# Performance work log

Measured on AMD Instinct MI355X. Metric: run time of the kernel, lower is better.

## Reference

```python
import jax, jax.numpy as jnp
import numpy as np

EPS = 1e-5

def layernorm(x, g, b):
    mu = jnp.mean(x, axis=-1, keepdims=True)
    var = jnp.mean(jnp.square(x - mu), axis=-1, keepdims=True)
    return (x - mu) * jax.lax.rsqrt(var + EPS) * g + b

def setup_inputs() -> dict:
    key = jax.random.key(0)
    ks = jax.random.split(key, 12)
    B, V, P, C = 2, 8192, 16, 256
    FFN_IN, FFN_HID = 2 * C, 2 * C * 4
    s = 0.02
    return {
        "source": jax.random.normal(ks[0], (B, V, C), jnp.float32),
        "target": jax.random.normal(ks[1], (B, V, P, C), jnp.float32),
        "weights": jax.random.uniform(ks[2], (B, V, P), jnp.float32),
        "confidences": jax.random.uniform(ks[3], (B, V, P), jnp.float32),
        "Wq": jax.random.normal(ks[4], (C, C), jnp.float32) * s,
        "Wk": jax.random.normal(ks[5], (C, C), jnp.float32) * s,
        "Wv": jax.random.normal(ks[6], (C, C), jnp.float32) * s,
        "Wm": jax.random.normal(ks[7], (C, C), jnp.float32) * s,
        "g1": jnp.ones((C,), jnp.float32),
        "b1": jnp.zeros((C,), jnp.float32),
        "Wf1": jax.random.normal(ks[8], (FFN_IN, FFN_HID), jnp.float32) * s,
        "Wf2": jax.random.normal(ks[9], (FFN_HID, C), jnp.float32) * s,
        "g2": jnp.ones((C,), jnp.float32),
        "b2": jnp.zeros((C,), jnp.float32),
    }

NUM_HEAD = 8

def reference(source, target, weights, confidences, Wq, Wk, Wv, Wm, g1, b1, Wf1, Wf2, g2, b2):
    B, V, P, C = target.shape
    H = NUM_HEAD
    D = C // H
    # projections (bias-free linears)
    q = (source @ Wq).reshape(B, V, H, D)          # [B,V,H,D]
    k = (target @ Wk).reshape(B, V, P, H, D)       # [B,V,P,H,D]
    v = (target @ Wv).reshape(B, V, P, H, D)
    # scores scaled by per-neighbor weights then softmax over P
    scores = jnp.einsum("bvhd,bvphd->bvhp", q, k) * weights[:, :, None, :] / jnp.sqrt(jnp.float32(D))
    attn = jax.nn.softmax(scores, axis=-1)          # [B,V,H,P]
    # confidence-scaled weighted sum over neighbors
    out = jnp.einsum("bvhp,bvp,bvphd->bvhd", attn, confidences, v).reshape(B, V, C)
    message = layernorm(out @ Wm, g1, b1)
    h = jnp.concatenate([source, message], axis=-1) @ Wf1
    message = layernorm(jax.nn.gelu(h, approximate=False) @ Wf2, g2, b2)
    return source + message
```

## Files before the change

### kernel.cpp

```cpp
#include <hip/hip_runtime.h>
#include <hip/hip_bf16.h>
#include <math.h>

#define T_TOK 16384
#define CC 256
#define PP 16
#define HH 8
#define DD 32
#define LN_EPS 1e-5f

typedef __attribute__((ext_vector_type(8))) short bf16x8_t;
typedef __attribute__((ext_vector_type(4))) float f32x4_t;

__device__ __forceinline__ unsigned short f2bf(float x) {
  __hip_bfloat16 h = __float2bfloat16(x);
  return *reinterpret_cast<unsigned short*>(&h);
}
__device__ __forceinline__ float bf2f(unsigned short u) {
  union { unsigned int i; float f; } v; v.i = ((unsigned int)u) << 16; return v.f;
}
__device__ __forceinline__ void gl_lds16(const unsigned short* g, unsigned short* l) {
  __builtin_amdgcn_global_load_lds(
      (const __attribute__((address_space(1))) unsigned int*)g,
      (__attribute__((address_space(3))) unsigned int*)l, 16, 0, 0);
}

__global__ __launch_bounds__(256) void cvt_bf16_kernel(const float* __restrict__ src,
                                                       unsigned short* __restrict__ dst) {
  int i = (blockIdx.x * 256 + threadIdx.x) * 4;
  float4 v = *(const float4*)&src[i];
  ushort4 o = make_ushort4(f2bf(v.x), f2bf(v.y), f2bf(v.z), f2bf(v.w));
  *(ushort4*)&dst[i] = o;
}

__global__ __launch_bounds__(256) void transpose_cvt_kernel(const float* __restrict__ src,
                                                            unsigned short* __restrict__ dst,
                                                            int K, int N) {
  __shared__ float tile[64][65];
  int k0 = blockIdx.x * 64, n0 = blockIdx.y * 64;
  int tid = threadIdx.x;
#pragma unroll
  for (int i = 0; i < 16; i++) {
    int lin = i * 256 + tid, r = lin >> 6, c = lin & 63;
    tile[r][c] = src[(size_t)(k0 + r) * N + n0 + c];
  }
  __syncthreads();
#pragma unroll
  for (int i = 0; i < 16; i++) {
    int lin = i * 256 + tid, n = lin >> 6, k = lin & 63;
    dst[(size_t)(n0 + n) * K + k0 + k] = f2bf(tile[k][n]);
  }
}

__global__ __launch_bounds__(256) void precM_kernel(const float* __restrict__ Wq,
                                                    const float* __restrict__ Wk,
                                                    unsigned short* __restrict__ Mt) {
  __shared__ float wqS[256][33];
  __shared__ float wkS[128][33];
  const int tid = threadIdx.x;
  const int h = blockIdx.x >> 1, eh = blockIdx.x & 1;
#pragma unroll
  for (int it = 0; it < 32; it++) {
    int lin = it * 256 + tid, r = lin >> 5, d = lin & 31;
    wqS[r][d] = Wq[(size_t)r * CC + h * DD + d];
  }
#pragma unroll
  for (int it = 0; it < 16; it++) {
    int lin = it * 256 + tid, r = lin >> 5, d = lin & 31;
    wkS[r][d] = Wk[(size_t)(eh * 128 + r) * CC + h * DD + d];
  }
  __syncthreads();
  const int w = tid >> 6, l = tid & 63;
  for (int ei = 0; ei < 32; ei++) {
    int e = w * 32 + ei;
    float o[4] = {0.f, 0.f, 0.f, 0.f};
#pragma unroll
    for (int d = 0; d < 32; d++) {
      float kv = wkS[e][d];
      o[0] += kv * wqS[l][d];
      o[1] += kv * wqS[l + 64][d];
      o[2] += kv * wqS[l + 128][d];
      o[3] += kv * wqS[l + 192][d];
    }
    size_t rowb = (size_t)(h * 256 + eh * 128 + e) * CC;
    Mt[rowb + l] = f2bf(o[0]);
    Mt[rowb + l + 64] = f2bf(o[1]);
    Mt[rowb + l + 128] = f2bf(o[2]);
    Mt[rowb + l + 192] = f2bf(o[3]);
  }
}

__global__ __launch_bounds__(256) void precWVM_kernel(const float* __restrict__ Wv,
                                                      const float* __restrict__ Wm,
                                                      unsigned short* __restrict__ WVMt) {
  __shared__ float WvS[256][33];
  __shared__ float WmS[32][257];
  const int h = blockIdx.x;
  const int tid = threadIdx.x;
#pragma unroll
  for (int it = 0; it < 32; it++) {
    int lin = it * 256 + tid, e = lin >> 5, d = lin & 31;
    WvS[e][d] = Wv[(size_t)e * CC + h * DD + d];
  }
#pragma unroll
  for (int it = 0; it < 32; it++) {
    int lin = it * 256 + tid, d = lin >> 8, c = lin & 255;
    WmS[d][c] = Wm[(size_t)(h * DD + d) * CC + c];
  }
  __syncthreads();
  float wm[32];
#pragma unroll
  for (int d = 0; d < 32; d++) wm[d] = WmS[d][tid];
  for (int e = 0; e < 256; e++) {
    float acc = 0.f;
#pragma unroll
    for (int d = 0; d < 32; d++) acc += WvS[e][d] * wm[d];
    WVMt[(size_t)tid * 2048 + h * 256 + e] = f2bf(acc);
  }
}

__global__ __launch_bounds__(512) void qk_gemm_kernel(
    const unsigned short* __restrict__ A, const unsigned short* __restrict__ Bt,
    unsigned short* __restrict__ Out, int K, int strideO) {
  __shared__ __align__(16) unsigned short As[64 * 32];
  __shared__ __align__(16) unsigned short Bs[256 * 32];
  const int tid = threadIdx.x;
  const int wv = tid >> 6, l = tid & 63;
  const int wr = wv >> 2, wc = wv & 3;
  const int lr = l & 15, lq = l >> 4;
  const int m0 = blockIdx.x * 64;
  const int n0 = blockIdx.y * 256;
  const int nsteps = K >> 5;

  f32x4_t acc[2][4];
#pragma unroll
  for (int m = 0; m < 2; m++)
#pragma unroll
    for (int n = 0; n < 4; n++) acc[m][n] = (f32x4_t){0.f, 0.f, 0.f, 0.f};

  const int rA = tid >> 2, sA = tid & 3, qA = sA ^ ((rA >> 1) & 3);

  for (int st = 0; st < nsteps; st++) {
    int kn = st * 32;
    if (tid < 256) gl_lds16(&A[(size_t)(m0 + rA) * K + kn + qA * 8], &As[tid * 8]);
#pragma unroll
    for (int it = 0; it < 2; it++) {
      int lin = it * 512 + tid, r = lin >> 2, s = lin & 3, q = s ^ ((r >> 1) & 3);
      gl_lds16(&Bt[(size_t)(n0 + r) * K + kn + q * 8], &Bs[lin * 8]);
    }
    __syncthreads();
    bf16x8_t af[2], bfr[4];
#pragma unroll
    for (int m = 0; m < 2; m++) {
      int r = wr * 32 + m * 16 + lr;
      int s = lq ^ ((r >> 1) & 3);
      af[m] = *(const bf16x8_t*)&As[r * 32 + s * 8];
    }
#pragma unroll
    for (int n = 0; n < 4; n++) {
      int r = wc * 64 + n * 16 + lr;
      int s = lq ^ ((r >> 1) & 3);
      bfr[n] = *(const bf16x8_t*)&Bs[r * 32 + s * 8];
    }
#pragma unroll
    for (int m = 0; m < 2; m++)
#pragma unroll
      for (int n = 0; n < 4; n++)
        acc[m][n] = __builtin_amdgcn_mfma_f32_16x16x32_bf16(af[m], bfr[n], acc[m][n], 0, 0, 0);
    __syncthreads();
  }

#pragma unroll
  for (int m = 0; m < 2; m++)
#pragma unroll
    for (int n = 0; n < 4; n++)
#pragma unroll
      for (int j = 0; j < 4; j++) {
        int rl = wr * 32 + m * 16 + lq * 4 + j;
        int col = n0 + wc * 64 + n * 16 + lr;
        Out[(size_t)(m0 + rl) * strideO + col] = f2bf(acc[m][n][j]);
      }
}

__global__ __launch_bounds__(256) void attn2_kernel(const unsigned short* __restrict__ QKc,
                                                    const float* __restrict__ target,
                                                    const float* __restrict__ wts,
                                                    const float* __restrict__ conf,
                                                    unsigned short* __restrict__ TC) {
  __shared__ __align__(16) unsigned short Ts[4][16 * 256];
  __shared__ float awL[4][PP][HH];
  const int tid = threadIdx.x;
  const int w = tid >> 6, l = tid & 63;
  const int t = blockIdx.x * 4 + w;
  const float* trow = target + (size_t)t * PP * CC;
  char* tsb = (char*)&Ts[w][0];

  {
    const int p = l >> 2;
#pragma unroll
    for (int i = 0; i < 8; i++) {
      int s = (l & 3) + i * 4;
      const float* gp = &trow[p * CC + s * 8];
      float4 v0 = *(const float4*)gp;
      float4 v1 = *(const float4*)(gp + 4);
      ushort4 u0 = make_ushort4(f2bf(v0.x), f2bf(v0.y), f2bf(v0.z), f2bf(v0.w));
      ushort4 u1 = make_ushort4(f2bf(v1.x), f2bf(v1.y), f2bf(v1.z), f2bf(v1.w));
      uint4 pk;
      pk.x = (unsigned)u0.x | ((unsigned)u0.y << 16);
      pk.y = (unsigned)u0.z | ((unsigned)u0.w << 16);
      pk.z = (unsigned)u1.x | ((unsigned)u1.y << 16);
      pk.w = (unsigned)u1.z | ((unsigned)u1.w << 16);
      *(uint4*)(tsb + p * 512 + ((s ^ (p & 7)) << 4)) = pk;
    }
  }

  f32x4_t sc4 = (f32x4_t){0.f, 0.f, 0.f, 0.f};
  {
    const int lr = l & 15, lq = l >> 4;
    const unsigned short* qkrow = QKc + (size_t)t * 2048 + (size_t)(lr & 7) * 256;
#pragma unroll
    for (int es = 0; es < 8; es++) {
      int slot = es * 4 + lq;
      bf16x8_t aF = *(const bf16x8_t*)(tsb + lr * 512 + ((slot ^ (lr & 7)) << 4));
      bf16x8_t bF = *(const bf16x8_t*)&qkrow[es * 32 + lq * 8];
      sc4 = __builtin_amdgcn_mfma_f32_16x16x32_bf16(aF, bF, sc4, 0, 0, 0);
    }
  }

  {
    const int g = l >> 4;
    const float rsD = 0.17677669529663687f;
    float sc[4], cf[4];
#pragma unroll
    for (int j = 0; j < 4; j++) {
      int p = g * 4 + j;
      sc[j] = sc4[j] * wts[(size_t)t * PP + p] * rsD;
      cf[j] = conf[(size_t)t * PP + p];
    }
    float mx = fmaxf(fmaxf(sc[0], sc[1]), fmaxf(sc[2], sc[3]));
    mx = fmaxf(mx, __shfl_xor(mx, 16, 64));
    mx = fmaxf(mx, __shfl_xor(mx, 32, 64));
    float ex[4], sm = 0.f;
#pragma unroll
    for (int j = 0; j < 4; j++) { ex[j] = expf(sc[j] - mx); sm += ex[j]; }
    sm += __shfl_xor(sm, 16, 64);
    sm += __shfl_xor(sm, 32, 64);
    float inv = 1.f / sm;
    if ((l & 15) < 8) {
#pragma unroll
      for (int j = 0; j < 4; j++) awL[w][g * 4 + j][l & 15] = ex[j] * inv * cf[j];
    }
  }

  float tc[HH][4];
#pragma unroll
  for (int h = 0; h < HH; h++)
#pragma unroll
    for (int j = 0; j < 4; j++) tc[h][j] = 0.f;
#pragma unroll
  for (int p = 0; p < PP; p++) {
    uint2 tv = *(const uint2*)(tsb + p * 512 + (((l >> 1) ^ (p & 7)) << 4) + (l & 1) * 8);
    float te0 = bf2f((unsigned short)(tv.x & 0xffff));
    float te1 = bf2f((unsigned short)(tv.x >> 16));
    float te2 = bf2f((unsigned short)(tv.y & 0xffff));
    float te3 = bf2f((unsigned short)(tv.y >> 16));
#pragma unroll
    for (int h = 0; h < HH; h++) {
      float a = awL[w][p][h];
      tc[h][0] += a * te0; tc[h][1] += a * te1;
      tc[h][2] += a * te2; tc[h][3] += a * te3;
    }
  }
  size_t tcb = (size_t)t * 2048;
#pragma unroll
  for (int h = 0; h < HH; h++) {
    ushort4 o = make_ushort4(f2bf(tc[h][0]), f2bf(tc[h][1]), f2bf(tc[h][2]), f2bf(tc[h][3]));
    *(ushort4*)&TC[tcb + h * 2048 / HH + 4 * l] = o;
  }
}

template<int EPI>
__global__ __launch_bounds__(256) void nwide_gemm_kernel(
    const unsigned short* __restrict__ A, const unsigned short* __restrict__ Bt,
    unsigned short* __restrict__ OutB, float* __restrict__ OutF,
    const float* __restrict__ gam, const float* __restrict__ bet,
    const float* __restrict__ res) {
  __shared__ __align__(16) unsigned short As[32 * 32];
  __shared__ __align__(16) unsigned short Bs[256 * 32];
  __shared__ float redS[32][5], redQ[32][5];
  const int tid = threadIdx.x;
  const int wc = tid >> 6, l = tid & 63;
  const int lr = l & 15, lq = l >> 4;
  const int m0 = blockIdx.x * 32;
  const int K = 2048;

  f32x4_t acc[2][4];
#pragma unroll
  for (int m = 0; m < 2; m++)
#pragma unroll
    for (int n = 0; n < 4; n++) acc[m][n] = (f32x4_t){0.f, 0.f, 0.f, 0.f};

  const int rA = tid >> 2, sA = tid & 3, qA = sA ^ ((rA >> 1) & 3);

  for (int st = 0; st < 64; st++) {
    int kn = st * 32;
    if (tid < 128) gl_lds16(&A[(size_t)(m0 + rA) * K + kn + qA * 8], &As[tid * 8]);
#pragma unroll
    for (int it = 0; it < 4; it++) {
      int lin = it * 256 + tid, r = lin >> 2, s = lin & 3, q = s ^ ((r >> 1) & 3);
      gl_lds16(&Bt[(size_t)r * K + kn + q * 8], &Bs[lin * 8]);
    }
    __syncthreads();
    bf16x8_t af[2], bfr[4];
#pragma unroll
    for (int m = 0; m < 2; m++) {
      int r = m * 16 + lr;
      int s = lq ^ ((r >> 1) & 3);
      af[m] = *(const bf16x8_t*)&As[r * 32 + s * 8];
    }
#pragma unroll
    for (int n = 0; n < 4; n++) {
      int r = wc * 64 + n * 16 + lr;
      int s = lq ^ ((r >> 1) & 3);
      bfr[n] = *(const bf16x8_t*)&Bs[r * 32 + s * 8];
    }
#pragma unroll
    for (int m = 0; m < 2; m++)
#pragma unroll
      for (int n = 0; n < 4; n++)
        acc[m][n] = __builtin_amdgcn_mfma_f32_16x16x32_bf16(af[m], bfr[n], acc[m][n], 0, 0, 0);
    __syncthreads();
  }

  float s1[2][4], s2[2][4];
#pragma unroll
  for (int m = 0; m < 2; m++)
#pragma unroll
    for (int j = 0; j < 4; j++) {
      float a = 0.f, b = 0.f;
#pragma unroll
      for (int n = 0; n < 4; n++) { float x = acc[m][n][j]; a += x; b += x * x; }
      s1[m][j] = a; s2[m][j] = b;
    }
#pragma unroll
  for (int mask = 1; mask < 16; mask <<= 1)
#pragma unroll
    for (int m = 0; m < 2; m++)
#pragma unroll
      for (int j = 0; j < 4; j++) {
        s1[m][j] += __shfl_xor(s1[m][j], mask, 64);
        s2[m][j] += __shfl_xor(s2[m][j], mask, 64);
      }
  if (lr == 0) {
#pragma unroll
    for (int m = 0; m < 2; m++)
#pragma unroll
      for (int j = 0; j < 4; j++) {
        int rl = m * 16 + lq * 4 + j;
        redS[rl][wc] = s1[m][j];
        redQ[rl][wc] = s2[m][j];
      }
  }
  __syncthreads();
#pragma unroll
  for (int m = 0; m < 2; m++)
#pragma unroll
    for (int j = 0; j < 4; j++) {
      int rl = m * 16 + lq * 4 + j;
      float ts = redS[rl][0] + redS[rl][1] + redS[rl][2] + redS[rl][3];
      float tq = redQ[rl][0] + redQ[rl][1] + redQ[rl][2] + redQ[rl][3];
      float mu = ts * (1.f / 256.f);
      float var = tq * (1.f / 256.f) - mu * mu;
      float rs = rsqrtf(var + LN_EPS);
      size_t rowg = (size_t)(m0 + rl);
#pragma unroll
      for (int n = 0; n < 4; n++) {
        int col = wc * 64 + n * 16 + lr;
        float v = (acc[m][n][j] - mu) * rs * gam[col] + bet[col];
        if constexpr (EPI == 0) {
          OutB[rowg * CC + col] = f2bf(v);
        } else {
          OutF[rowg * CC + col] = res[rowg * CC + col] + v;
        }
      }
    }
}

__global__ __launch_bounds__(256) void gemm1_kernel(
    const unsigned short* __restrict__ SB, const unsigned short* __restrict__ MSG,
    const unsigned short* __restrict__ W1t, unsigned short* __restrict__ hid) {
  __shared__ __align__(16) unsigned short As[128 * 32];
  __shared__ __align__(16) unsigned short Bs[128 * 32];
  const int tid = threadIdx.x;
  const int wv = tid >> 6, l = tid & 63;
  const int wr = wv >> 1, wc = wv & 1;
  const int lr = l & 15, lq = l >> 4;
  const int m0 = blockIdx.x * 128;
  const int n0 = blockIdx.y * 128;

  f32x4_t acc[4][4];
#pragma unroll
  for (int m = 0; m < 4; m++)
#pragma unroll
    for (int n = 0; n < 4; n++) acc[m][n] = (f32x4_t){0.f, 0.f, 0.f, 0.f};

  for (int st = 0; st < 16; st++) {
    int kn = st * 32;
#pragma unroll
    for (int it = 0; it < 2; it++) {
      int lin = it * 256 + tid, r = lin >> 2, s = lin & 3, q = s ^ ((r >> 1) & 3);
      int ka = kn + q * 8;
      const unsigned short* ap = (ka < 256) ? &SB[(size_t)(m0 + r) * CC + ka]
                                            : &MSG[(size_t)(m0 + r) * CC + ka - 256];
      gl_lds16(ap, &As[lin * 8]);
      gl_lds16(&W1t[(size_t)(n0 + r) * 512 + kn + q * 8], &Bs[lin * 8]);
    }
    __syncthreads();
    bf16x8_t af[4], bf[4];
#pragma unroll
    for (int m = 0; m < 4; m++) {
      int r = wr * 64 + m * 16 + lr;
      int s = lq ^ ((r >> 1) & 3);
      af[m] = *(const bf16x8_t*)&As[r * 32 + s * 8];
    }
#pragma unroll
    for (int n = 0; n < 4; n++) {
      int r = wc * 64 + n * 16 + lr;
      int s = lq ^ ((r >> 1) & 3);
      bf[n] = *(const bf16x8_t*)&Bs[r * 32 + s * 8];
    }
#pragma unroll
    for (int m = 0; m < 4; m++)
#pragma unroll
      for (int n = 0; n < 4; n++)
        acc[m][n] = __builtin_amdgcn_mfma_f32_16x16x32_bf16(af[m], bf[n], acc[m][n], 0, 0, 0);
    __syncthreads();
  }

#pragma unroll
  for (int m = 0; m < 4; m++)
#pragma unroll
    for (int n = 0; n < 4; n++)
#pragma unroll
      for (int j = 0; j < 4; j++) {
        int row = m0 + wr * 64 + m * 16 + lq * 4 + j;
        int col = n0 + wc * 64 + n * 16 + lr;
        float x = acc[m][n][j];
        float gl = 0.5f * x * (1.0f + erff(x * 0.70710678118654752f));
        hid[(size_t)row * 2048 + col] = f2bf(gl);
      }
}

extern "C" void kernel_launch(void* const* d_in, const int* in_sizes, int n_in,
                              void* d_out, int out_size, void* d_ws, size_t ws_size,
                              hipStream_t stream) {
  const float* source = (const float*)d_in[0];
  const float* target = (const float*)d_in[1];
  const float* weights = (const float*)d_in[2];
  const float* conf   = (const float*)d_in[3];
  const float* Wq = (const float*)d_in[4];
  const float* Wk = (const float*)d_in[5];
  const float* Wv = (const float*)d_in[6];
  const float* Wm = (const float*)d_in[7];
  const float* g1 = (const float*)d_in[8];
  const float* b1 = (const float*)d_in[9];
  const float* Wf1 = (const float*)d_in[10];
  const float* Wf2 = (const float*)d_in[11];
  const float* g2 = (const float*)d_in[12];
  const float* b2 = (const float*)d_in[13];
  float* out = (float*)d_out;

  unsigned short* SB   = (unsigned short*)d_ws;
  unsigned short* MSGb = SB + (size_t)T_TOK * CC;
  unsigned short* Mt   = MSGb + (size_t)T_TOK * CC;
  unsigned short* WVMt = Mt + (size_t)2048 * 256;
  unsigned short* WF1t = WVMt + (size_t)256 * 2048;
  unsigned short* WF2t = WF1t + (size_t)2048 * 512;
  unsigned short* BIG1 = WF2t + (size_t)256 * 2048;
  unsigned short* BIG2 = BIG1 + (size_t)T_TOK * 2048;
  unsigned short* QKc  = BIG1;
  unsigned short* hid  = BIG1;
  unsigned short* TC   = BIG2;

  cvt_bf16_kernel<<<T_TOK * CC / 1024, 256, 0, stream>>>(source, SB);
  transpose_cvt_kernel<<<dim3(8, 32), 256, 0, stream>>>(Wf1, WF1t, 512, 2048);
  transpose_cvt_kernel<<<dim3(32, 4), 256, 0, stream>>>(Wf2, WF2t, 2048, 256);
  precM_kernel<<<16, 256, 0, stream>>>(Wq, Wk, Mt);
  precWVM_kernel<<<8, 256, 0, stream>>>(Wv, Wm, WVMt);

  qk_gemm_kernel<<<dim3(T_TOK / 64, 8), 512, 0, stream>>>(SB, Mt, QKc, 256, 2048);
  attn2_kernel<<<T_TOK / 4, 256, 0, stream>>>(QKc, target, weights, conf, TC);
  nwide_gemm_kernel<0><<<T_TOK / 32, 256, 0, stream>>>(
      TC, WVMt, MSGb, nullptr, g1, b1, nullptr);

  gemm1_kernel<<<dim3(T_TOK / 128, 16), 256, 0, stream>>>(SB, MSGb, WF1t, hid);
  nwide_gemm_kernel<1><<<T_TOK / 32, 256, 0, stream>>>(
      hid, WF2t, nullptr, out, g2, b2, source);
}
```

Baseline: 359.7 us.

## Double-buffer LDS tiles in the three GEMM kernels to overlap loads with MFMA

Converts the qk, nwide and gemm1 GEMM main loops to ping-pong LDS buffers, prefetching the next K-slice via global_load_lds while MFMAs consume the current one, with a prologue load of the first slice. This targets the exposed global-load latency of the single-buffered load→sync→compute→sync loop. It doubles LDS use per block, which can lower occupancy, and relies on the remaining end-of-iteration barrier to keep the buffers safe. A TC store index is also rewritten to an equivalent constant form.

```diff
diff --git a/kernel.cpp b/kernel.cpp
--- a/kernel.cpp
+++ b/kernel.cpp
@@ -122,8 +122,8 @@
 __global__ __launch_bounds__(512) void qk_gemm_kernel(
     const unsigned short* __restrict__ A, const unsigned short* __restrict__ Bt,
     unsigned short* __restrict__ Out, int K, int strideO) {
-  __shared__ __align__(16) unsigned short As[64 * 32];
-  __shared__ __align__(16) unsigned short Bs[256 * 32];
+  __shared__ __align__(16) unsigned short As[2][64 * 32];
+  __shared__ __align__(16) unsigned short Bs[2][256 * 32];
   const int tid = threadIdx.x;
   const int wv = tid >> 6, l = tid & 63;
   const int wr = wv >> 2, wc = wv & 3;
@@ -140,27 +140,37 @@
 
   const int rA = tid >> 2, sA = tid & 3, qA = sA ^ ((rA >> 1) & 3);
 
+  if (tid < 256) gl_lds16(&A[(size_t)(m0 + rA) * K + qA * 8], &As[0][tid * 8]);
+#pragma unroll
+  for (int it = 0; it < 2; it++) {
+    int lin = it * 512 + tid, r = lin >> 2, s = lin & 3, q = s ^ ((r >> 1) & 3);
+    gl_lds16(&Bt[(size_t)(n0 + r) * K + q * 8], &Bs[0][lin * 8]);
+  }
+  __syncthreads();
+
   for (int st = 0; st < nsteps; st++) {
-    int kn = st * 32;
-    if (tid < 256) gl_lds16(&A[(size_t)(m0 + rA) * K + kn + qA * 8], &As[tid * 8]);
-#pragma unroll
-    for (int it = 0; it < 2; it++) {
-      int lin = it * 512 + tid, r = lin >> 2, s = lin & 3, q = s ^ ((r >> 1) & 3);
-      gl_lds16(&Bt[(size_t)(n0 + r) * K + kn + q * 8], &Bs[lin * 8]);
-    }
-    __syncthreads();
+    int cur = st & 1;
+    if (st + 1 < nsteps) {
+      int kn = (st + 1) * 32;
+      if (tid < 256) gl_lds16(&A[(size_t)(m0 + rA) * K + kn + qA * 8], &As[cur ^ 1][tid * 8]);
+#pragma unroll
+      for (int it = 0; it < 2; it++) {
+        int lin = it * 512 + tid, r = lin >> 2, s = lin & 3, q = s ^ ((r >> 1) & 3);
+        gl_lds16(&Bt[(size_t)(n0 + r) * K + kn + q * 8], &Bs[cur ^ 1][lin * 8]);
+      }
+    }
     bf16x8_t af[2], bfr[4];
 #pragma unroll
     for (int m = 0; m < 2; m++) {
       int r = wr * 32 + m * 16 + lr;
       int s = lq ^ ((r >> 1) & 3);
-      af[m] = *(const bf16x8_t*)&As[r * 32 + s * 8];
+      af[m] = *(const bf16x8_t*)&As[cur][r * 32 + s * 8];
     }
 #pragma unroll
     for (int n = 0; n < 4; n++) {
       int r = wc * 64 + n * 16 + lr;
       int s = lq ^ ((r >> 1) & 3);
-      bfr[n] = *(const bf16x8_t*)&Bs[r * 32 + s * 8];
+      bfr[n] = *(const bf16x8_t*)&Bs[cur][r * 32 + s * 8];
     }
 #pragma unroll
     for (int m = 0; m < 2; m++)
@@ -275,7 +285,7 @@
 #pragma unroll
   for (int h = 0; h < HH; h++) {
     ushort4 o = make_ushort4(f2bf(tc[h][0]), f2bf(tc[h][1]), f2bf(tc[h][2]), f2bf(tc[h][3]));
-    *(ushort4*)&TC[tcb + h * 2048 / HH + 4 * l] = o;
+    *(ushort4*)&TC[tcb + h * 256 + 4 * l] = o;
   }
 }
 
@@ -285,8 +295,8 @@
     unsigned short* __restrict__ OutB, float* __restrict__ OutF,
     const float* __restrict__ gam, const float* __restrict__ bet,
     const float* __restrict__ res) {
-  __shared__ __align__(16) unsigned short As[32 * 32];
-  __shared__ __align__(16) unsigned short Bs[256 * 32];
+  __shared__ __align__(16) unsigned short As[2][32 * 32];
+  __shared__ __align__(16) unsigned short Bs[2][256 * 32];
   __shared__ float redS[32][5], redQ[32][5];
   const int tid = threadIdx.x;
   const int wc = tid >> 6, l = tid & 63;
@@ -302,27 +312,37 @@
 
   const int rA = tid >> 2, sA = tid & 3, qA = sA ^ ((rA >> 1) & 3);
 
+  if (tid < 128) gl_lds16(&A[(size_t)(m0 + rA) * K + qA * 8], &As[0][tid * 8]);
+#pragma unroll
+  for (int it = 0; it < 4; it++) {
+    int lin = it * 256 + tid, r = lin >> 2, s = lin & 3, q = s ^ ((r >> 1) & 3);
+    gl_lds16(&Bt[(size_t)r * K + q * 8], &Bs[0][lin * 8]);
+  }
+  __syncthreads();
+
   for (int st = 0; st < 64; st++) {
-    int kn = st * 32;
-    if (tid < 128) gl_lds16(&A[(size_t)(m0 + rA) * K + kn + qA * 8], &As[tid * 8]);
-#pragma unroll
-    for (int it = 0; it < 4; it++) {
-      int lin = it * 256 + tid, r = lin >> 2, s = lin & 3, q = s ^ ((r >> 1) & 3);
-      gl_lds16(&Bt[(size_t)r * K + kn + q * 8], &Bs[lin * 8]);
-    }
-    __syncthreads();
+    int cur = st & 1;
+    if (st < 63) {
+      int kn = (st + 1) * 32;
+      if (tid < 128) gl_lds16(&A[(size_t)(m0 + rA) * K + kn + qA * 8], &As[cur ^ 1][tid * 8]);
+#pragma unroll
+      for (int it = 0; it < 4; it++) {
+        int lin = it * 256 + tid, r = lin >> 2, s = lin & 3, q = s ^ ((r >> 1) & 3);
+        gl_lds16(&Bt[(size_t)r * K + kn + q * 8], &Bs[cur ^ 1][lin * 8]);
+      }
+    }
     bf16x8_t af[2], bfr[4];
 #pragma unroll
     for (int m = 0; m < 2; m++) {
       int r = m * 16 + lr;
       int s = lq ^ ((r >> 1) & 3);
-      af[m] = *(const bf16x8_t*)&As[r * 32 + s * 8];
+      af[m] = *(const bf16x8_t*)&As[cur][r * 32 + s * 8];
     }
 #pragma unroll
     for (int n = 0; n < 4; n++) {
       int r = wc * 64 + n * 16 + lr;
       int s = lq ^ ((r >> 1) & 3);
-      bfr[n] = *(const bf16x8_t*)&Bs[r * 32 + s * 8];
+      bfr[n] = *(const bf16x8_t*)&Bs[cur][r * 32 + s * 8];
     }
 #pragma unroll
     for (int m = 0; m < 2; m++)
@@ -389,8 +409,8 @@
 __global__ __launch_bounds__(256) void gemm1_kernel(
     const unsigned short* __restrict__ SB, const unsigned short* __restrict__ MSG,
     const unsigned short* __restrict__ W1t, unsigned short* __restrict__ hid) {
-  __shared__ __align__(16) unsigned short As[128 * 32];
-  __shared__ __align__(16) unsigned short Bs[128 * 32];
+  __shared__ __align__(16) unsigned short As[2][128 * 32];
+  __shared__ __align__(16) unsigned short Bs[2][128 * 32];
   const int tid = threadIdx.x;
   const int wv = tid >> 6, l = tid & 63;
   const int wr = wv >> 1, wc = wv & 1;
@@ -404,30 +424,40 @@
 #pragma unroll
     for (int n = 0; n < 4; n++) acc[m][n] = (f32x4_t){0.f, 0.f, 0.f, 0.f};
 
+#pragma unroll
+  for (int it = 0; it < 2; it++) {
+    int lin = it * 256 + tid, r = lin >> 2, s = lin & 3, q = s ^ ((r >> 1) & 3);
+    gl_lds16(&SB[(size_t)(m0 + r) * CC + q * 8], &As[0][lin * 8]);
+    gl_lds16(&W1t[(size_t)(n0 + r) * 512 + q * 8], &Bs[0][lin * 8]);
+  }
+  __syncthreads();
+
   for (int st = 0; st < 16; st++) {
-    int kn = st * 32;
-#pragma unroll
-    for (int it = 0; it < 2; it++) {
-      int lin = it * 256 + tid, r = lin >> 2, s = lin & 3, q = s ^ ((r >> 1) & 3);
-      int ka = kn + q * 8;
-      const unsigned short* ap = (ka < 256) ? &SB[(size_t)(m0 + r) * CC + ka]
-                                            : &MSG[(size_t)(m0 + r) * CC + ka - 256];
-      gl_lds16(ap, &As[lin * 8]);
-      gl_lds16(&W1t[(size_t)(n0 + r) * 512 + kn + q * 8], &Bs[lin * 8]);
-    }
-    __syncthreads();
+    int cur = st & 1;
+    if (st < 15) {
+      int kn = (st + 1) * 32;
+#pragma unroll
+      for (int it = 0; it < 2; it++) {
+        int lin = it * 256 + tid, r = lin >> 2, s = lin & 3, q = s ^ ((r >> 1) & 3);
+        int ka = kn + q * 8;
+        const unsigned short* ap = (ka < 256) ? &SB[(size_t)(m0 + r) * CC + ka]
+                                              : &MSG[(size_t)(m0 + r) * CC + ka - 256];
+        gl_lds16(ap, &As[cur ^ 1][lin * 8]);
+        gl_lds16(&W1t[(size_t)(n0 + r) * 512 + kn + q * 8], &Bs[cur ^ 1][lin * 8]);
+      }
+    }
     bf16x8_t af[4], bf[4];
 #pragma unroll
     for (int m = 0; m < 4; m++) {
       int r = wr * 64 + m * 16 + lr;
       int s = lq ^ ((r >> 1) & 3);
-      af[m] = *(const bf16x8_t*)&As[r * 32 + s * 8];
+      af[m] = *(const bf16x8_t*)&As[cur][r * 32 + s * 8];
     }
 #pragma unroll
     for (int n = 0; n < 4; n++) {
       int r = wc * 64 + n * 16 + lr;
       int s = lq ^ ((r >> 1) & 3);
-      bf[n] = *(const bf16x8_t*)&Bs[r * 32 + s * 8];
+      bf[n] = *(const bf16x8_t*)&Bs[cur][r * 32 + s * 8];
     }
 #pragma unroll
     for (int m = 0; m < 4; m++)
```

Result: slower. 368.3 us (+2.4%).
